# Kernel optimization log

Measured on AMD Instinct MI355X. Metric: run time of the kernel, lower is better.

The kernel has to match this reference:

```python
import jax, jax.numpy as jnp
import numpy as np

N = 50000   # total nodes (50 graphs x 1000 nodes)
E = 500000  # total edges (avg degree 10)
G = 50      # number of graphs in the batch
IN = 128    # in_dim
H = 4       # attn_head
HID = [64, 128]  # graph_hiddens
SLOPE = 0.2      # negative_slope


def setup_inputs() -> dict:
    key = jax.random.key(0)
    ks = jax.random.split(key, 12)
    nodes_per_g = N // G
    edges_per_g = E // G
    # edges stay inside their own graph block (batched-graph structure)
    off = (jnp.arange(E) // edges_per_g) * nodes_per_g
    edge_src = (jax.random.randint(ks[0], (E,), 0, nodes_per_g) + off).astype(jnp.int32)
    edge_dst = (jax.random.randint(ks[1], (E,), 0, nodes_per_g) + off).astype(jnp.int32)
    node_graph = (jnp.arange(N) // nodes_per_g).astype(jnp.int32)

    def lin(k, i, o):
        return (jax.random.normal(k, (i, o), jnp.float32) / np.sqrt(i)).astype(jnp.float32)

    return dict(
        x=jax.random.normal(ks[2], (N, IN), jnp.float32),
        edge_src=edge_src, edge_dst=edge_dst, node_graph=node_graph,
        Wl1=lin(ks[3], IN, H * HID[0]), bl1=jnp.zeros((H * HID[0],), jnp.float32),
        Wr1=lin(ks[4], IN, H * HID[0]), br1=jnp.zeros((H * HID[0],), jnp.float32),
        attn1=jax.random.normal(ks[5], (H, HID[0]), jnp.float32) * 0.1,
        Wl2=lin(ks[6], HID[0], H * HID[1]), bl2=jnp.zeros((H * HID[1],), jnp.float32),
        Wr2=lin(ks[7], HID[0], H * HID[1]), br2=jnp.zeros((H * HID[1],), jnp.float32),
        attn2=jax.random.normal(ks[8], (H, HID[1]), jnp.float32) * 0.1,
        gate_w=lin(ks[9], HID[1], 1), gate_b=jnp.zeros((1,), jnp.float32),
    )


def _gat_layer(x, src, dst, Wl, bl, Wr, br, attn, n_heads, d_out):
    """DGL GATv2Conv (share_weights=False, no dropout) + maxpool over heads."""
    n = x.shape[0]
    fs = (x @ Wl + bl).reshape(n, n_heads, d_out)  # fc_src -> [N,H,D]
    fd = (x @ Wr + br).reshape(n, n_heads, d_out)  # fc_dst -> [N,H,D]
    # per-edge GATv2 logits: attn . leaky_relu(fs_u + fd_v)
    e = jax.nn.leaky_relu(fs[src] + fd[dst], SLOPE)      # [E,H,D]
    logits = jnp.einsum('ehd,hd->eh', e, attn)           # [E,H]
    # edge softmax over incoming edges of each destination node
    m = jax.ops.segment_max(logits, dst, num_segments=n)  # [N,H]
    a = jnp.exp(logits - m[dst])
    s = jax.ops.segment_sum(a, dst, num_segments=n)
    alpha = a / s[dst]                                   # [E,H]
    out = jax.ops.segment_sum(alpha[:, :, None] * fs[src], dst, num_segments=n)  # [N,H,D]
    # MaxPool1d(attn_head) over the head dimension -> [N,D]
    return out.max(axis=1)


def reference(x, edge_src, edge_dst, node_graph,
              Wl1, bl1, Wr1, br1, attn1,
              Wl2, bl2, Wr2, br2, attn2,
              gate_w, gate_b):
    h = _gat_layer(x, edge_src, edge_dst, Wl1, bl1, Wr1, br1, attn1, H, HID[0])
    h = _gat_layer(h, edge_src, edge_dst, Wl2, bl2, Wr2, br2, attn2, H, HID[1])
    # GlobalAttentionPooling: softmax(gate_nn(h)) per graph, weighted sum
    gate = (h @ gate_w + gate_b)[:, 0]                      # [N]
    gm = jax.ops.segment_max(gate, node_graph, num_segments=G)
    ga = jnp.exp(gate - gm[node_graph])
    gs = jax.ops.segment_sum(ga, node_graph, num_segments=G)
    alpha = (ga / gs[node_graph])[:, None]                  # [N,1]
    return jax.ops.segment_sum(alpha * h, node_graph, num_segments=G)  # [G, HID[1]]
```

## Files before the change

### kernel.cpp

```cpp
#include <hip/hip_runtime.h>
#include <hip/hip_bf16.h>


#define NN 50000
#define EE 500000
#define GG 50
#define NPG 1000
#define HH 4
#define NB_E ((EE + 255) / 256)
#define NB_W 512

typedef unsigned short ushort_t;
typedef unsigned int uint_t;
typedef __attribute__((ext_vector_type(8))) short bf16x8;
typedef __attribute__((ext_vector_type(4))) float f32x4;
typedef __attribute__((ext_vector_type(2))) float f32x2;

__device__ __forceinline__ ushort_t bf16r(float f) {
  __hip_bfloat16 h = __float2bfloat16(f);
  return *reinterpret_cast<ushort_t*>(&h);
}

__device__ __forceinline__ f32x2 up2v(uint_t u) {
  f32x2 r;
  r.x = __uint_as_float(u << 16);
  r.y = __uint_as_float(u & 0xffff0000u);
  return r;
}


__global__ void prep_count(const int* __restrict__ dst, int* __restrict__ counts,
                           const float* __restrict__ Wl1, const float* __restrict__ Wr1,
                           const float* __restrict__ Wl2, const float* __restrict__ Wr2,
                           ushort_t* __restrict__ BW1, ushort_t* __restrict__ BW2) {
  const int b = blockIdx.x;
  if (b < NB_E) {
    int i = b * 256 + threadIdx.x;
    if (i < EE) atomicAdd(&counts[dst[i]], 1);
  } else {
    int i = (b - NB_E) * 256 + threadIdx.x;
    if (i < 512 * 128) {
      int n = i >> 7, k = i & 127;
      const float* W = (n < 256) ? Wl1 : Wr1;
      BW1[i] = bf16r(W[(size_t)k * 256 + (n & 255)]);
    } else {
      int j = i - 512 * 128;
      int n = j >> 6, k = j & 63;
      const float* W = (n < 512) ? Wl2 : Wr2;
      BW2[j] = bf16r(W[(size_t)k * 512 + (n & 511)]);
    }
  }
}


__global__ void scan_block(const int* __restrict__ in, int* __restrict__ out,
                           int* __restrict__ bsum, int n) {
  __shared__ int tmp[256];
  int t = threadIdx.x;
  int i = blockIdx.x * 256 + t;
  int v = (i < n) ? in[i] : 0;
  tmp[t] = v;
  __syncthreads();
  for (int off = 1; off < 256; off <<= 1) {
    int a = (t >= off) ? tmp[t - off] : 0;
    __syncthreads();
    tmp[t] += a;
    __syncthreads();
  }
  if (i < n) out[i] = tmp[t] - v;
  if (t == 255) bsum[blockIdx.x] = tmp[t];
}

__global__ void scan_bsum(int* __restrict__ bsum, int nb) {
  __shared__ int tmp[256];
  int t = threadIdx.x;
  int v = (t < nb) ? bsum[t] : 0;
  tmp[t] = v;
  __syncthreads();
  for (int off = 1; off < 256; off <<= 1) {
    int a = (t >= off) ? tmp[t - off] : 0;
    __syncthreads();
    tmp[t] += a;
    __syncthreads();
  }
  if (t < nb) bsum[t] = tmp[t] - v;
}

__global__ void scan_add(int* __restrict__ out, const int* __restrict__ bsum,
                         int* __restrict__ cursor, int n) {
  int i = blockIdx.x * 256 + threadIdx.x;
  if (i < n) {
    out[i] += bsum[blockIdx.x];
    cursor[i] = 0;
  }
}

__global__ void scatter_edges(const int* __restrict__ src, const int* __restrict__ dst,
                              const int* __restrict__ rowstart, int* __restrict__ cursor,
                              int* __restrict__ csr_src) {
  int i = blockIdx.x * 256 + threadIdx.x;
  if (i < EE) {
    int d = dst[i];
    int p = atomicAdd(&cursor[d], 1);
    csr_src[rowstart[d] + p] = src[i];
  }
}


template<int KDIM, bool AF32>
__global__ __launch_bounds__(256)
void gemm_mfma(const float* __restrict__ Af, const ushort_t* __restrict__ Ab,
               const ushort_t* __restrict__ BW,
               const float* __restrict__ bl, const float* __restrict__ br, int nhalf,
               ushort_t* __restrict__ C, int nstride) {
  constexpr int RS  = 72;
  constexpr int EPS = 132;
  __shared__ __align__(16) ushort_t smem[2 * 128 * RS];
  ushort_t* As = smem;
  ushort_t* Bs = smem + 128 * RS;
  const int t = threadIdx.x;
  const int m0 = blockIdx.x * 128, n0 = blockIdx.y * 128;
  const int lane = t & 63, wv = t >> 6;
  const int l16 = lane & 15, quad = lane >> 4;

  f32x4 acc[2][8];
#pragma unroll
  for (int b = 0; b < 2; ++b)
#pragma unroll
    for (int n = 0; n < 8; ++n) acc[b][n] = (f32x4){0.f, 0.f, 0.f, 0.f};

  for (int k0 = 0; k0 < KDIM; k0 += 64) {
    __syncthreads();
    if (AF32) {
      const int r = t >> 4, c4 = t & 15;
#pragma unroll
      for (int p = 0; p < 8; ++p) {
        int m = m0 + r + p * 16;
        int ms = (m < NN) ? m : NN - 1;
        float4 v = *(const float4*)(Af + (size_t)ms * KDIM + k0 + c4 * 4);
        uint2 pk;
        pk.x = (uint_t)bf16r(v.x) | ((uint_t)bf16r(v.y) << 16);
        pk.y = (uint_t)bf16r(v.z) | ((uint_t)bf16r(v.w) << 16);
        *(uint2*)(As + (r + p * 16) * RS + c4 * 4) = pk;
      }
    } else {
      const int r = t >> 3, seg = t & 7;
#pragma unroll
      for (int p = 0; p < 4; ++p) {
        int m = m0 + r + p * 32;
        int ms = (m < NN) ? m : NN - 1;
        *(uint4*)(As + (r + p * 32) * RS + seg * 8) =
            *(const uint4*)(Ab + (size_t)ms * KDIM + k0 + seg * 8);
      }
    }
    {
      const int r = t >> 3, seg = t & 7;
#pragma unroll
      for (int p = 0; p < 4; ++p) {
        *(uint4*)(Bs + (r + p * 32) * RS + seg * 8) =
            *(const uint4*)(BW + (size_t)(n0 + r + p * 32) * KDIM + k0 + seg * 8);
      }
    }
    __syncthreads();
#pragma unroll
    for (int kk = 0; kk < 2; ++kk) {
      bf16x8 a[2];
#pragma unroll
      for (int b = 0; b < 2; ++b)
        a[b] = *(const bf16x8*)(As + (wv * 32 + b * 16 + l16) * RS + kk * 32 + quad * 8);
#pragma unroll
      for (int n = 0; n < 8; ++n) {
        bf16x8 bb = *(const bf16x8*)(Bs + (n * 16 + l16) * RS + kk * 32 + quad * 8);
        acc[0][n] = __builtin_amdgcn_mfma_f32_16x16x32_bf16(a[0], bb, acc[0][n], 0, 0, 0);
        acc[1][n] = __builtin_amdgcn_mfma_f32_16x16x32_bf16(a[1], bb, acc[1][n], 0, 0, 0);
      }
    }
  }

  __syncthreads();
  ushort_t* band = smem + wv * 32 * EPS;
  const float* bp = (n0 < nhalf) ? bl : br;
  const int nb = (n0 < nhalf) ? n0 : n0 - nhalf;
#pragma unroll
  for (int n = 0; n < 8; ++n) {
    const float bv = bp[nb + n * 16 + l16];
#pragma unroll
    for (int b = 0; b < 2; ++b)
#pragma unroll
      for (int r = 0; r < 4; ++r)
        band[(b * 16 + quad * 4 + r) * EPS + n * 16 + l16] = bf16r(acc[b][n][r] + bv);
  }
  const int rl   = lane >> 4;
  const int cseg = lane & 15;
#pragma unroll
  for (int g = 0; g < 8; ++g) {
    const int row_local = g * 4 + rl;
    const int row = m0 + wv * 32 + row_local;
    uint4 vx = *(const uint4*)(band + row_local * EPS + cseg * 8);
    if (row < NN)
      *(uint4*)(C + (size_t)row * nstride + n0 + cseg * 8) = vx;
  }
}


template<int N32> struct UV;
template<> struct UV<2> { typedef uint2 T; };
template<> struct UV<4> { typedef uint4 T; };

#define GAT_SLOTS ((NN / 4 + 7) / 8)
#define GAT_GRID  (GAT_SLOTS * 8)

template<int D, int STRIDE, bool OUTBF, bool GATE>
__global__ __launch_bounds__(256)
void gat_layer(const ushort_t* __restrict__ fsb, const ushort_t* __restrict__ fdb,
               const float* __restrict__ attn,
               const int* __restrict__ rowstart, const int* __restrict__ deg,
               const int* __restrict__ csr_src,
               float4* __restrict__ out4, ushort_t* __restrict__ outb,
               const float* __restrict__ gw, float* __restrict__ gate) {
  constexpr int DPL = D / 16;
  constexpr int NU  = DPL / 2;
  constexpr int NV4 = DPL / 4;
  constexpr int D4  = D / 4;
  typedef typename UV<NU>::T LT;

  const int b    = blockIdx.x;
  const int slot = (b & 7) * GAT_SLOTS + (b >> 3);
  if (slot >= NN / 4) return;
  const int lane = threadIdx.x & 63;
  const int wvid = threadIdx.x >> 6;
  const int v    = (slot << 2) + wvid;
  const int h    = lane >> 4;
  const int g16  = lane & 15;
  const int foff = h * D + g16 * DPL;

  f32x2 at2[NU], fd2[NU];
  {
    const float* ap = attn + foff;
#pragma unroll
    for (int j = 0; j < NU; ++j) {
      at2[j].x = ap[2 * j] * 1.44269504f;
      at2[j].y = ap[2 * j + 1] * 1.44269504f;
    }
    LT raw = *reinterpret_cast<const LT*>(fdb + (size_t)v * STRIDE + foff);
    const uint_t* rw = reinterpret_cast<const uint_t*>(&raw);
#pragma unroll
    for (int j = 0; j < NU; ++j) fd2[j] = up2v(rw[j]);
  }
  const int start = __builtin_amdgcn_readfirstlane(rowstart[v]);
  const int n     = __builtin_amdgcn_readfirstlane(deg[v]);
  const int* cp   = csr_src + start;

  float s = 0.f;
  f32x2 acc2[NU];
#pragma unroll
  for (int j = 0; j < NU; ++j) acc2[j] = (f32x2){0.f, 0.f};

  if (n > 0) {
    LT r0 = *reinterpret_cast<const LT*>(fsb + (size_t)cp[0] * STRIDE + foff);
    LT r1 = r0;
    if (n > 1)
      r1 = *reinterpret_cast<const LT*>(fsb + (size_t)cp[1] * STRIDE + foff);
    for (int e = 0; e < n; ++e) {
      const LT cur = r0;
      r0 = r1;
      if (e + 2 < n)
        r1 = *reinterpret_cast<const LT*>(fsb + (size_t)cp[e + 2] * STRIDE + foff);
      const uint_t* rw = reinterpret_cast<const uint_t*>(&cur);
      f32x2 f0[NU];
#pragma unroll
      for (int j = 0; j < NU; ++j) f0[j] = up2v(rw[j]);
      f32x2 p2 = (f32x2){0.f, 0.f};
#pragma unroll
      for (int j = 0; j < NU; ++j) {
        f32x2 t = f0[j] + fd2[j];
        f32x2 l = __builtin_elementwise_max(t, t * 0.2f);
        p2 = __builtin_elementwise_fma(l, at2[j], p2);
      }
      float p = p2.x + p2.y;
      p += __shfl_xor(p, 1);
      p += __shfl_xor(p, 2);
      p += __shfl_xor(p, 4);
      p += __shfl_xor(p, 8);
      const float w = exp2f(p);
      s += w;
      const f32x2 wv2 = {w, w};
#pragma unroll
      for (int j = 0; j < NU; ++j)
        acc2[j] = __builtin_elementwise_fma(wv2, f0[j], acc2[j]);
    }
  }

  const float rs = (n > 0) ? (1.0f / s) : 0.f;
  float acc[DPL];
#pragma unroll
  for (int j = 0; j < NU; ++j) {
    acc[2 * j]     = acc2[j].x * rs;
    acc[2 * j + 1] = acc2[j].y * rs;
  }
#pragma unroll
  for (int i = 0; i < DPL; ++i) {
    acc[i] = fmaxf(acc[i], __shfl_xor(acc[i], 16));
    acc[i] = fmaxf(acc[i], __shfl_xor(acc[i], 32));
  }
  if constexpr (GATE) {
    const float* gp = gw + g16 * DPL;
    float g = 0.f;
#pragma unroll
    for (int i = 0; i < DPL; ++i) g = fmaf(acc[i], gp[i], g);
    g += __shfl_xor(g, 1);  g += __shfl_xor(g, 2);  g += __shfl_xor(g, 4);
    g += __shfl_xor(g, 8);  g += __shfl_xor(g, 16); g += __shfl_xor(g, 32);
    if (lane == 0) gate[v] = g * 0.25f;
  }
  if (h == 0) {
    if constexpr (OUTBF) {
      ushort4 o;
      o.x = bf16r(acc[0]); o.y = bf16r(acc[1]); o.z = bf16r(acc[2]); o.w = bf16r(acc[3]);
      *reinterpret_cast<ushort4*>(outb + (size_t)v * D + g16 * 4) = o;
    } else {
#pragma unroll
      for (int i = 0; i < NV4; ++i)
        out4[(size_t)v * D4 + g16 * NV4 + i] =
            make_float4(acc[4 * i], acc[4 * i + 1], acc[4 * i + 2], acc[4 * i + 3]);
    }
  }
}


__global__ __launch_bounds__(1024)
void pool_fused(const float* __restrict__ gate, const float* __restrict__ h2,
                float* __restrict__ out) {
  const int g = blockIdx.x, t = threadIdx.x;
  const int lane = t & 63, w = t >> 6;
  __shared__ float a_s[NPG];
  __shared__ float red[16];
  __shared__ float fin;
  __shared__ float part[8][128];

  float gv = (t < NPG) ? gate[g * NPG + t] : -__builtin_inff();
  float m = gv;
  m = fmaxf(m, __shfl_xor(m, 1));  m = fmaxf(m, __shfl_xor(m, 2));
  m = fmaxf(m, __shfl_xor(m, 4));  m = fmaxf(m, __shfl_xor(m, 8));
  m = fmaxf(m, __shfl_xor(m, 16)); m = fmaxf(m, __shfl_xor(m, 32));
  if (lane == 0) red[w] = m;
  __syncthreads();
  if (t == 0) {
    float r = red[0];
#pragma unroll
    for (int j = 1; j < 16; ++j) r = fmaxf(r, red[j]);
    fin = r;
  }
  __syncthreads();
  const float gm = fin;

  float ex = (t < NPG) ? __expf(gv - gm) : 0.f;
  float s = ex;
  s += __shfl_xor(s, 1);  s += __shfl_xor(s, 2);  s += __shfl_xor(s, 4);
  s += __shfl_xor(s, 8);  s += __shfl_xor(s, 16); s += __shfl_xor(s, 32);
  if (lane == 0) red[w] = s;
  __syncthreads();
  if (t == 0) {
    float r = 0.f;
#pragma unroll
    for (int j = 0; j < 16; ++j) r += red[j];
    fin = 1.0f / r;
  }
  __syncthreads();
  if (t < NPG) a_s[t] = ex * fin;
  __syncthreads();

  const int d = t & 127;
  const int c = t >> 7;
  float acc = 0.f;
  for (int i = c; i < NPG; i += 8)
    acc = fmaf(a_s[i], h2[(size_t)(g * NPG + i) * 128 + d], acc);
  part[c][d] = acc;
  __syncthreads();
  if (c == 0) {
    float r = acc;
#pragma unroll
    for (int j = 1; j < 8; ++j) r += part[j][d];
    out[g * 128 + d] = r;
  }
}


extern "C" void kernel_launch(void* const* d_in, const int* in_sizes, int n_in,
                              void* d_out, int out_size, void* d_ws, size_t ws_size,
                              hipStream_t stream) {
  const float* x        = (const float*)d_in[0];
  const int*   edge_src = (const int*)d_in[1];
  const int*   edge_dst = (const int*)d_in[2];
  const float* Wl1   = (const float*)d_in[4];
  const float* bl1   = (const float*)d_in[5];
  const float* Wr1   = (const float*)d_in[6];
  const float* br1   = (const float*)d_in[7];
  const float* attn1 = (const float*)d_in[8];
  const float* Wl2   = (const float*)d_in[9];
  const float* bl2   = (const float*)d_in[10];
  const float* Wr2   = (const float*)d_in[11];
  const float* br2   = (const float*)d_in[12];
  const float* attn2 = (const float*)d_in[13];
  const float* gate_w = (const float*)d_in[14];
  float* out = (float*)d_out;

  ushort_t* fsd1 = (ushort_t*)d_ws;
  ushort_t* fsd2 = fsd1;
  ushort_t* h1b  = fsd2 + (size_t)NN * 1024;
  float* h2      = (float*)(h1b + (size_t)NN * 64);
  float* gate    = h2 + (size_t)NN * 128;
  ushort_t* BW1  = (ushort_t*)(gate + NN);
  ushort_t* BW2  = BW1 + 512 * 128;
  int* counts   = (int*)(BW2 + 1024 * 64);
  int* rowstart = counts + NN;
  int* cursor   = rowstart + NN;
  int* csr_src  = cursor + NN;
  int* bsum     = csr_src + EE;

  hipMemsetAsync(counts, 0, NN * sizeof(int), stream);

  const int nbN = (NN + 255) / 256;
  const int nbE = NB_E;
  const int MB  = (NN + 127) / 128;

  prep_count<<<NB_E + NB_W, 256, 0, stream>>>(
      edge_dst, counts, Wl1, Wr1, Wl2, Wr2, BW1, BW2);
  scan_block<<<nbN, 256, 0, stream>>>(counts, rowstart, bsum, NN);
  scan_bsum<<<1, 256, 0, stream>>>(bsum, nbN);
  scan_add<<<nbN, 256, 0, stream>>>(rowstart, bsum, cursor, NN);
  scatter_edges<<<nbE, 256, 0, stream>>>(edge_src, edge_dst, rowstart, cursor, csr_src);

  gemm_mfma<128, true><<<dim3(MB, 4), 256, 0, stream>>>(
      x, nullptr, BW1, bl1, br1, 256, fsd1, 512);
  gat_layer<64, 512, true, false><<<GAT_GRID, 256, 0, stream>>>(
      fsd1, fsd1 + 256, attn1, rowstart, counts, csr_src,
      nullptr, h1b, nullptr, nullptr);
  gemm_mfma<64, false><<<dim3(MB, 8), 256, 0, stream>>>(
      nullptr, h1b, BW2, bl2, br2, 512, fsd2, 1024);
  gat_layer<128, 1024, false, true><<<GAT_GRID, 256, 0, stream>>>(
      fsd2, fsd2 + 512, attn2, rowstart, counts, csr_src,
      (float4*)h2, nullptr, gate_w, gate);

  pool_fused<<<GG, 1024, 0, stream>>>(gate, h2, out);
}
```

Measured before the change: 338.8 us.

## Pre-convert x to bf16, fold scan_bsum into scan_add, loop GAT slots per block

The fp32-to-bf16 conversion of x moves out of the first GEMM into the prep kernel, so each GEMM N-tile block no longer re-converts the fp32 A rows. The separate single-block bsum scan is dropped: each scan_add block sums the preceding block totals itself with wave reductions, which removes one launch. GAT blocks now process four node slots each in a loop, keeping the XCD-interleaved mapping and cutting block count. The costs are an extra bf16 copy of x written to and read from memory, redundant bsum reads in every scan_add block, and fewer blocks to hide latency in the GAT kernels.

```diff
diff --git a/kernel.cpp b/kernel.cpp
--- a/kernel.cpp
+++ b/kernel.cpp
@@ -9,6 +9,7 @@
 #define HH 4
 #define NB_E ((EE + 255) / 256)
 #define NB_W 512
+#define NB_X ((NN * 128) / (256 * 4))
 
 typedef unsigned short ushort_t;
 typedef unsigned int uint_t;
@@ -32,12 +33,13 @@
 __global__ void prep_count(const int* __restrict__ dst, int* __restrict__ counts,
                            const float* __restrict__ Wl1, const float* __restrict__ Wr1,
                            const float* __restrict__ Wl2, const float* __restrict__ Wr2,
-                           ushort_t* __restrict__ BW1, ushort_t* __restrict__ BW2) {
+                           ushort_t* __restrict__ BW1, ushort_t* __restrict__ BW2,
+                           const float* __restrict__ x, ushort_t* __restrict__ xb) {
   const int b = blockIdx.x;
   if (b < NB_E) {
     int i = b * 256 + threadIdx.x;
     if (i < EE) atomicAdd(&counts[dst[i]], 1);
-  } else {
+  } else if (b < NB_E + NB_W) {
     int i = (b - NB_E) * 256 + threadIdx.x;
     if (i < 512 * 128) {
       int n = i >> 7, k = i & 127;
@@ -49,6 +51,13 @@
       const float* W = (n < 512) ? Wl2 : Wr2;
       BW2[j] = bf16r(W[(size_t)k * 512 + (n & 511)]);
     }
+  } else {
+    size_t i = (size_t)(b - NB_E - NB_W) * 256 + threadIdx.x;
+    float4 v = *(const float4*)(x + i * 4);
+    uint2 pk;
+    pk.x = (uint_t)bf16r(v.x) | ((uint_t)bf16r(v.y) << 16);
+    pk.y = (uint_t)bf16r(v.z) | ((uint_t)bf16r(v.w) << 16);
+    *(uint2*)(xb + i * 4) = pk;
   }
 }
 
@@ -71,26 +80,20 @@
   if (t == 255) bsum[blockIdx.x] = tmp[t];
 }
 
-__global__ void scan_bsum(int* __restrict__ bsum, int nb) {
-  __shared__ int tmp[256];
-  int t = threadIdx.x;
-  int v = (t < nb) ? bsum[t] : 0;
-  tmp[t] = v;
-  __syncthreads();
-  for (int off = 1; off < 256; off <<= 1) {
-    int a = (t >= off) ? tmp[t - off] : 0;
-    __syncthreads();
-    tmp[t] += a;
-    __syncthreads();
-  }
-  if (t < nb) bsum[t] = tmp[t] - v;
-}
-
-__global__ void scan_add(int* __restrict__ out, const int* __restrict__ bsum,
+__global__ void scan_add(const int* __restrict__ bsum, int* __restrict__ out,
                          int* __restrict__ cursor, int n) {
-  int i = blockIdx.x * 256 + threadIdx.x;
+  __shared__ int sred[4];
+  const int t = threadIdx.x;
+  const int b = blockIdx.x;
+  int v = (t < b) ? bsum[t] : 0;
+  v += __shfl_xor(v, 1);  v += __shfl_xor(v, 2);  v += __shfl_xor(v, 4);
+  v += __shfl_xor(v, 8);  v += __shfl_xor(v, 16); v += __shfl_xor(v, 32);
+  if ((t & 63) == 0) sred[t >> 6] = v;
+  __syncthreads();
+  const int base = sred[0] + sred[1] + sred[2] + sred[3];
+  int i = b * 256 + t;
   if (i < n) {
-    out[i] += bsum[blockIdx.x];
+    out[i] += base;
     cursor[i] = 0;
   }
 }
@@ -107,10 +110,9 @@
 }
 
 
-template<int KDIM, bool AF32>
+template<int KDIM>
 __global__ __launch_bounds__(256)
-void gemm_mfma(const float* __restrict__ Af, const ushort_t* __restrict__ Ab,
-               const ushort_t* __restrict__ BW,
+void gemm_mfma(const ushort_t* __restrict__ Ab, const ushort_t* __restrict__ BW,
                const float* __restrict__ bl, const float* __restrict__ br, int nhalf,
                ushort_t* __restrict__ C, int nstride) {
   constexpr int RS  = 72;
@@ -131,19 +133,7 @@
 
   for (int k0 = 0; k0 < KDIM; k0 += 64) {
     __syncthreads();
-    if (AF32) {
-      const int r = t >> 4, c4 = t & 15;
-#pragma unroll
-      for (int p = 0; p < 8; ++p) {
-        int m = m0 + r + p * 16;
-        int ms = (m < NN) ? m : NN - 1;
-        float4 v = *(const float4*)(Af + (size_t)ms * KDIM + k0 + c4 * 4);
-        uint2 pk;
-        pk.x = (uint_t)bf16r(v.x) | ((uint_t)bf16r(v.y) << 16);
-        pk.y = (uint_t)bf16r(v.z) | ((uint_t)bf16r(v.w) << 16);
-        *(uint2*)(As + (r + p * 16) * RS + c4 * 4) = pk;
-      }
-    } else {
+    {
       const int r = t >> 3, seg = t & 7;
 #pragma unroll
       for (int p = 0; p < 4; ++p) {
@@ -151,12 +141,6 @@
         int ms = (m < NN) ? m : NN - 1;
         *(uint4*)(As + (r + p * 32) * RS + seg * 8) =
             *(const uint4*)(Ab + (size_t)ms * KDIM + k0 + seg * 8);
-      }
-    }
-    {
-      const int r = t >> 3, seg = t & 7;
-#pragma unroll
-      for (int p = 0; p < 4; ++p) {
         *(uint4*)(Bs + (r + p * 32) * RS + seg * 8) =
             *(const uint4*)(BW + (size_t)(n0 + r + p * 32) * KDIM + k0 + seg * 8);
       }
@@ -207,8 +191,9 @@
 template<> struct UV<2> { typedef uint2 T; };
 template<> struct UV<4> { typedef uint4 T; };
 
-#define GAT_SLOTS ((NN / 4 + 7) / 8)
-#define GAT_GRID  (GAT_SLOTS * 8)
+#define GAT_SLOTS 1563
+#define GAT_BLKX  ((GAT_SLOTS + 3) / 4)
+#define GAT_GRID  (GAT_BLKX * 8)
 
 template<int D, int STRIDE, bool OUTBF, bool GATE>
 __global__ __launch_bounds__(256)
@@ -225,16 +210,15 @@
   typedef typename UV<NU>::T LT;
 
   const int b    = blockIdx.x;
-  const int slot = (b & 7) * GAT_SLOTS + (b >> 3);
-  if (slot >= NN / 4) return;
+  const int xcd  = b & 7;
+  const int bi   = b >> 3;
   const int lane = threadIdx.x & 63;
   const int wvid = threadIdx.x >> 6;
-  const int v    = (slot << 2) + wvid;
   const int h    = lane >> 4;
   const int g16  = lane & 15;
   const int foff = h * D + g16 * DPL;
 
-  f32x2 at2[NU], fd2[NU];
+  f32x2 at2[NU];
   {
     const float* ap = attn + foff;
 #pragma unroll
@@ -242,86 +226,98 @@
       at2[j].x = ap[2 * j] * 1.44269504f;
       at2[j].y = ap[2 * j + 1] * 1.44269504f;
     }
-    LT raw = *reinterpret_cast<const LT*>(fdb + (size_t)v * STRIDE + foff);
-    const uint_t* rw = reinterpret_cast<const uint_t*>(&raw);
-#pragma unroll
-    for (int j = 0; j < NU; ++j) fd2[j] = up2v(rw[j]);
-  }
-  const int start = __builtin_amdgcn_readfirstlane(rowstart[v]);
-  const int n     = __builtin_amdgcn_readfirstlane(deg[v]);
-  const int* cp   = csr_src + start;
-
-  float s = 0.f;
-  f32x2 acc2[NU];
-#pragma unroll
-  for (int j = 0; j < NU; ++j) acc2[j] = (f32x2){0.f, 0.f};
-
-  if (n > 0) {
-    LT r0 = *reinterpret_cast<const LT*>(fsb + (size_t)cp[0] * STRIDE + foff);
-    LT r1 = r0;
-    if (n > 1)
-      r1 = *reinterpret_cast<const LT*>(fsb + (size_t)cp[1] * STRIDE + foff);
-    for (int e = 0; e < n; ++e) {
-      const LT cur = r0;
-      r0 = r1;
-      if (e + 2 < n)
-        r1 = *reinterpret_cast<const LT*>(fsb + (size_t)cp[e + 2] * STRIDE + foff);
-      const uint_t* rw = reinterpret_cast<const uint_t*>(&cur);
-      f32x2 f0[NU];
-#pragma unroll
-      for (int j = 0; j < NU; ++j) f0[j] = up2v(rw[j]);
-      f32x2 p2 = (f32x2){0.f, 0.f};
-#pragma unroll
-      for (int j = 0; j < NU; ++j) {
-        f32x2 t = f0[j] + fd2[j];
-        f32x2 l = __builtin_elementwise_max(t, t * 0.2f);
-        p2 = __builtin_elementwise_fma(l, at2[j], p2);
+  }
+
+  for (int jj = 0; jj < 4; ++jj) {
+    const int si = bi * 4 + jj;
+    if (si >= GAT_SLOTS) break;
+    const int slot = xcd * GAT_SLOTS + si;
+    if (slot >= NN / 4) break;
+    const int v = (slot << 2) + wvid;
+
+    f32x2 fd2[NU];
+    {
+      LT raw = *reinterpret_cast<const LT*>(fdb + (size_t)v * STRIDE + foff);
+      const uint_t* rw = reinterpret_cast<const uint_t*>(&raw);
+#pragma unroll
+      for (int j = 0; j < NU; ++j) fd2[j] = up2v(rw[j]);
+    }
+    const int start = __builtin_amdgcn_readfirstlane(rowstart[v]);
+    const int n     = __builtin_amdgcn_readfirstlane(deg[v]);
+    const int* cp   = csr_src + start;
+
+    float s = 0.f;
+    f32x2 acc2[NU];
+#pragma unroll
+    for (int j = 0; j < NU; ++j) acc2[j] = (f32x2){0.f, 0.f};
+
+    if (n > 0) {
+      LT r0 = *reinterpret_cast<const LT*>(fsb + (size_t)cp[0] * STRIDE + foff);
+      LT r1 = r0;
+      if (n > 1)
+        r1 = *reinterpret_cast<const LT*>(fsb + (size_t)cp[1] * STRIDE + foff);
+      for (int e = 0; e < n; ++e) {
+        const LT cur = r0;
+        r0 = r1;
+        if (e + 2 < n)
+          r1 = *reinterpret_cast<const LT*>(fsb + (size_t)cp[e + 2] * STRIDE + foff);
+        const uint_t* rw = reinterpret_cast<const uint_t*>(&cur);
+        f32x2 f0[NU];
+#pragma unroll
+        for (int j = 0; j < NU; ++j) f0[j] = up2v(rw[j]);
+        f32x2 p2 = (f32x2){0.f, 0.f};
+#pragma unroll
+        for (int j = 0; j < NU; ++j) {
+          f32x2 t = f0[j] + fd2[j];
+          f32x2 l = __builtin_elementwise_max(t, t * 0.2f);
+          p2 = __builtin_elementwise_fma(l, at2[j], p2);
+        }
+        float p = p2.x + p2.y;
+        p += __shfl_xor(p, 1);
+        p += __shfl_xor(p, 2);
+        p += __shfl_xor(p, 4);
+        p += __shfl_xor(p, 8);
+        const float w = exp2f(p);
+        s += w;
+        const f32x2 wv2 = {w, w};
+#pragma unroll
+        for (int j = 0; j < NU; ++j)
+          acc2[j] = __builtin_elementwise_fma(wv2, f0[j], acc2[j]);
       }
-      float p = p2.x + p2.y;
-      p += __shfl_xor(p, 1);
-      p += __shfl_xor(p, 2);
-      p += __shfl_xor(p, 4);
-      p += __shfl_xor(p, 8);
-      const float w = exp2f(p);
-      s += w;
-      const f32x2 wv2 = {w, w};
-#pragma unroll
-      for (int j = 0; j < NU; ++j)
-        acc2[j] = __builtin_elementwise_fma(wv2, f0[j], acc2[j]);
-    }
-  }
-
-  const float rs = (n > 0) ? (1.0f / s) : 0.f;
-  float acc[DPL];
-#pragma unroll
-  for (int j = 0; j < NU; ++j) {
-    acc[2 * j]     = acc2[j].x * rs;
-    acc[2 * j + 1] = acc2[j].y * rs;
-  }
-#pragma unroll
-  for (int i = 0; i < DPL; ++i) {
-    acc[i] = fmaxf(acc[i], __shfl_xor(acc[i], 16));
-    acc[i] = fmaxf(acc[i], __shfl_xor(acc[i], 32));
-  }
-  if constexpr (GATE) {
-    const float* gp = gw + g16 * DPL;
-    float g = 0.f;
-#pragma unroll
-    for (int i = 0; i < DPL; ++i) g = fmaf(acc[i], gp[i], g);
-    g += __shfl_xor(g, 1);  g += __shfl_xor(g, 2);  g += __shfl_xor(g, 4);
-    g += __shfl_xor(g, 8);  g += __shfl_xor(g, 16); g += __shfl_xor(g, 32);
-    if (lane == 0) gate[v] = g * 0.25f;
-  }
-  if (h == 0) {
-    if constexpr (OUTBF) {
-      ushort4 o;
-      o.x = bf16r(acc[0]); o.y = bf16r(acc[1]); o.z = bf16r(acc[2]); o.w = bf16r(acc[3]);
-      *reinterpret_cast<ushort4*>(outb + (size_t)v * D + g16 * 4) = o;
-    } else {
-#pragma unroll
-      for (int i = 0; i < NV4; ++i)
-        out4[(size_t)v * D4 + g16 * NV4 + i] =
-            make_float4(acc[4 * i], acc[4 * i + 1], acc[4 * i + 2], acc[4 * i + 3]);
+    }
+
+    const float rs = (n > 0) ? (1.0f / s) : 0.f;
+    float acc[DPL];
+#pragma unroll
+    for (int j = 0; j < NU; ++j) {
+      acc[2 * j]     = acc2[j].x * rs;
+      acc[2 * j + 1] = acc2[j].y * rs;
+    }
+#pragma unroll
+    for (int i = 0; i < DPL; ++i) {
+      acc[i] = fmaxf(acc[i], __shfl_xor(acc[i], 16));
+      acc[i] = fmaxf(acc[i], __shfl_xor(acc[i], 32));
+    }
+    if constexpr (GATE) {
+      const float* gp = gw + g16 * DPL;
+      float g = 0.f;
+#pragma unroll
+      for (int i = 0; i < DPL; ++i) g = fmaf(acc[i], gp[i], g);
+      g += __shfl_xor(g, 1);  g += __shfl_xor(g, 2);  g += __shfl_xor(g, 4);
+      g += __shfl_xor(g, 8);  g += __shfl_xor(g, 16); g += __shfl_xor(g, 32);
+      if (lane == 0) gate[v] = g * 0.25f;
+    }
+    if (h == 0) {
+      if constexpr (OUTBF) {
+        ushort4 o;
+        o.x = bf16r(acc[0]); o.y = bf16r(acc[1]); o.z = bf16r(acc[2]); o.w = bf16r(acc[3]);
+        *reinterpret_cast<ushort4*>(outb + (size_t)v * D + g16 * 4) = o;
+      } else {
+#pragma unroll
+        for (int i = 0; i < NV4; ++i)
+          out4[(size_t)v * D4 + g16 * NV4 + i] =
+              make_float4(acc[4 * i], acc[4 * i + 1], acc[4 * i + 2], acc[4 * i + 3]);
+      }
     }
   }
 }
@@ -411,7 +407,8 @@
   float* gate    = h2 + (size_t)NN * 128;
   ushort_t* BW1  = (ushort_t*)(gate + NN);
   ushort_t* BW2  = BW1 + 512 * 128;
-  int* counts   = (int*)(BW2 + 1024 * 64);
+  ushort_t* xb   = BW2 + 1024 * 64;
+  int* counts   = (int*)(xb + (size_t)NN * 128);
   int* rowstart = counts + NN;
   int* cursor   = rowstart + NN;
   int* csr_src  = cursor + NN;
@@ -420,23 +417,21 @@
   hipMemsetAsync(counts, 0, NN * sizeof(int), stream);
 
   const int nbN = (NN + 255) / 256;
-  const int nbE = NB_E;
   const int MB  = (NN + 127) / 128;
 
-  prep_count<<<NB_E + NB_W, 256, 0, stream>>>(
-      edge_dst, counts, Wl1, Wr1, Wl2, Wr2, BW1, BW2);
+  prep_count<<<NB_E + NB_W + NB_X, 256, 0, stream>>>(
+      edge_dst, counts, Wl1, Wr1, Wl2, Wr2, BW1, BW2, x, xb);
   scan_block<<<nbN, 256, 0, stream>>>(counts, rowstart, bsum, NN);
-  scan_bsum<<<1, 256, 0, stream>>>(bsum, nbN);
-  scan_add<<<nbN, 256, 0, stream>>>(rowstart, bsum, cursor, NN);
-  scatter_edges<<<nbE, 256, 0, stream>>>(edge_src, edge_dst, rowstart, cursor, csr_src);
-
-  gemm_mfma<128, true><<<dim3(MB, 4), 256, 0, stream>>>(
-      x, nullptr, BW1, bl1, br1, 256, fsd1, 512);
+  scan_add<<<nbN, 256, 0, stream>>>(bsum, rowstart, cursor, NN);
+  scatter_edges<<<NB_E, 256, 0, stream>>>(edge_src, edge_dst, rowstart, cursor, csr_src);
+
+  gemm_mfma<128><<<dim3(MB, 4), 256, 0, stream>>>(
+      xb, BW1, bl1, br1, 256, fsd1, 512);
   gat_layer<64, 512, true, false><<<GAT_GRID, 256, 0, stream>>>(
       fsd1, fsd1 + 256, attn1, rowstart, counts, csr_src,
       nullptr, h1b, nullptr, nullptr);
-  gemm_mfma<64, false><<<dim3(MB, 8), 256, 0, stream>>>(
-      nullptr, h1b, BW2, bl2, br2, 512, fsd2, 1024);
+  gemm_mfma<64><<<dim3(MB, 8), 256, 0, stream>>>(
+      h1b, BW2, bl2, br2, 512, fsd2, 1024);
   gat_layer<128, 1024, false, true><<<GAT_GRID, 256, 0, stream>>>(
       fsd2, fsd2 + 512, attn2, rowstart, counts, csr_src,
       (float4*)h2, nullptr, gate_w, gate);
```

Result: slower. 356.7 us (+5.3%).
